# Optimization experiments

Hardware: AMD Instinct MI355X
Metric: run time of the kernel (lower is better)

## Reference

```python
import jax, jax.numpy as jnp
import numpy as np
from jax import lax

WIN_SIZE = 11
WIN_SIGMA = 1.5
DATA_RANGE = 1.0
K1, K2 = 0.01, 0.03


def _gauss_1d(win_size, sigma):
    coords = jnp.arange(win_size, dtype=jnp.float32) - win_size // 2
    g = jnp.exp(-(coords ** 2) / (2.0 * sigma ** 2))
    return g / jnp.sum(g)


def _gauss_filter(x, win):
    # Separable depthwise gaussian blur, VALID padding (matches pytorch_msssim).
    C = x.shape[1]
    kh = jnp.tile(win.reshape(1, 1, -1, 1), (C, 1, 1, 1))  # (C,1,k,1)
    kw = jnp.tile(win.reshape(1, 1, 1, -1), (C, 1, 1, 1))  # (C,1,1,k)
    dn = ('NCHW', 'OIHW', 'NCHW')
    x = lax.conv_general_dilated(x, kh, (1, 1), 'VALID',
                                 dimension_numbers=dn, feature_group_count=C)
    x = lax.conv_general_dilated(x, kw, (1, 1), 'VALID',
                                 dimension_numbers=dn, feature_group_count=C)
    return x


def _ssim(X, Y, win, data_range):
    C1 = (K1 * data_range) ** 2
    C2 = (K2 * data_range) ** 2
    mu1 = _gauss_filter(X, win)
    mu2 = _gauss_filter(Y, win)
    mu1_sq = mu1 * mu1
    mu2_sq = mu2 * mu2
    mu1_mu2 = mu1 * mu2
    sigma1_sq = _gauss_filter(X * X, win) - mu1_sq
    sigma2_sq = _gauss_filter(Y * Y, win) - mu2_sq
    sigma12 = _gauss_filter(X * Y, win) - mu1_mu2
    cs_map = (2.0 * sigma12 + C2) / (sigma1_sq + sigma2_sq + C2)
    ssim_map = ((2.0 * mu1_mu2 + C1) / (mu1_sq + mu2_sq + C1)) * cs_map
    return jnp.mean(ssim_map)


def setup_inputs() -> dict:
    key = jax.random.key(0)
    k1, k2 = jax.random.split(key)
    shape = (16, 3, 384, 512)
    pred = jax.random.uniform(k1, shape, dtype=jnp.float32)
    target = jax.random.uniform(k2, shape, dtype=jnp.float32)
    return {"pred": pred, "target": target}


def reference(pred, target):
    win = _gauss_1d(WIN_SIZE, WIN_SIGMA)
    ssim_val = _ssim(pred, target, win, DATA_RANGE)
    return 1.0 - ssim_val
```

## Files before the change

### kernel.cpp

```cpp
#include <hip/hip_runtime.h>
#include <math.h>

#define WIN 11
#define IMG_H 384
#define IMG_W 512
#define OUT_H (IMG_H - WIN + 1)
#define OUT_W (IMG_W - WIN + 1)
#define RPW 2
#define NPAIRS 187
#define NIMG 48
#define TOTAL_PAIRS (NPAIRS * NIMG)
#define WPB 4
#define NBLOCKS 2248
#define BPX 281
#define NBUCKETS 256

typedef float v2 __attribute__((ext_vector_type(2)));

struct GaussW { float g[WIN]; };
struct Row { float4 xa, xb, ya, yb; };

__device__ __forceinline__ v2 shfl_v2(v2 v, int src) {
    v2 r; r.x = __shfl(v.x, src, 64); r.y = __shfl(v.y, src, 64); return r;
}

__device__ __forceinline__ void horiz11_v2(const v2 (&A)[8], v2 (&out)[8],
                                           int lane, const GaussW& gw)
{
    v2 V[18];
    #pragma unroll
    for (int j = 0; j < 8; ++j) V[j] = A[j];
    #pragma unroll
    for (int j = 0; j < 8; ++j) V[8 + j] = shfl_v2(A[j], lane + 1);
    V[16] = shfl_v2(A[0], lane + 2);
    V[17] = shfl_v2(A[1], lane + 2);
    #pragma unroll
    for (int j = 0; j < 8; ++j) {
        v2 o = 0.f;
        #pragma unroll
        for (int k = 0; k < WIN; ++k) {
            v2 g = gw.g[k];
            o = __builtin_elementwise_fma(g, V[j + k], o);
        }
        out[j] = o;
    }
}

__device__ __forceinline__ void horiz11_f(const float (&A)[8], float (&out)[8],
                                          int lane, const GaussW& gw)
{
    float V[18];
    #pragma unroll
    for (int j = 0; j < 8; ++j) V[j] = A[j];
    #pragma unroll
    for (int j = 0; j < 8; ++j) V[8 + j] = __shfl(A[j], lane + 1, 64);
    V[16] = __shfl(A[0], lane + 2, 64);
    V[17] = __shfl(A[1], lane + 2, 64);
    #pragma unroll
    for (int j = 0; j < 8; ++j) {
        float o = 0.f;
        #pragma unroll
        for (int k = 0; k < WIN; ++k) o = fmaf(gw.g[k], V[j + k], o);
        out[j] = o;
    }
}

__global__ __launch_bounds__(256) void ssim_fused_kernel(
    const float* __restrict__ X, const float* __restrict__ Y,
    double* __restrict__ accum, GaussW gw)
{
    const int wave = threadIdx.x >> 6;
    const int lane = threadIdx.x & 63;

    const int id = blockIdx.x;
    const int wb = (id & 7) * BPX + (id >> 3);
    const int P  = wb * WPB + wave;
    if (P >= TOTAL_PAIRS) return;

    const int img  = P / NPAIRS;
    const int pair = P % NPAIRS;
    const int r0   = pair * RPW;
    const int c0   = lane << 3;
    const float* __restrict__ Xb = X + ((size_t)img * IMG_H + r0) * IMG_W + c0;
    const float* __restrict__ Yb = Y + ((size_t)img * IMG_H + r0) * IMG_W + c0;

    v2 a01[RPW][8], a23[RPW][8];
    float a4[RPW][8];
    #pragma unroll
    for (int r = 0; r < RPW; ++r)
        #pragma unroll
        for (int j = 0; j < 8; ++j) { a01[r][j] = 0.f; a23[r][j] = 0.f; a4[r][j] = 0.f; }

    #define LOADROW(B, K) {                                                  \
        const float* _rx = Xb + (size_t)(K) * IMG_W;                         \
        const float* _ry = Yb + (size_t)(K) * IMG_W;                         \
        (B).xa = *(const float4*)(_rx);                                      \
        (B).xb = *(const float4*)(_rx + 4);                                  \
        (B).ya = *(const float4*)(_ry);                                      \
        (B).yb = *(const float4*)(_ry + 4);                                  \
    }

    Row buf[3];
    LOADROW(buf[0], 0); LOADROW(buf[1], 1); LOADROW(buf[2], 2);
    __builtin_amdgcn_sched_barrier(0);

    #pragma unroll
    for (int k = 0; k < RPW + WIN - 1; ++k) {
        Row cur = buf[k % 3];
        if (k + 3 < RPW + WIN - 1) LOADROW(buf[k % 3], k + 3);

        v2 p[8] = {{cur.xa.x, cur.ya.x}, {cur.xa.y, cur.ya.y},
                   {cur.xa.z, cur.ya.z}, {cur.xa.w, cur.ya.w},
                   {cur.xb.x, cur.yb.x}, {cur.xb.y, cur.yb.y},
                   {cur.xb.z, cur.yb.z}, {cur.xb.w, cur.yb.w}};
        #pragma unroll
        for (int r = 0; r < RPW; ++r) {
            if (k - r >= 0 && k - r < WIN) {
                v2 g = gw.g[k - r];
                #pragma unroll
                for (int j = 0; j < 8; ++j) {
                    v2 q = p[j];
                    a01[r][j] = __builtin_elementwise_fma(g, q, a01[r][j]);
                    v2 t = g * q;
                    a23[r][j] = __builtin_elementwise_fma(t, q, a23[r][j]);
                    a4[r][j]  = fmaf(t.x, q.y, a4[r][j]);
                }
            }
        }
        __builtin_amdgcn_sched_barrier(0);
    }
    #undef LOADROW

    const float C1 = 1e-4f, C2 = 9e-4f;
    float sum = 0.f;
    #pragma unroll
    for (int r = 0; r < RPW; ++r) {
        v2 h01[8], h23[8];
        float h4[8];
        horiz11_v2(a01[r], h01, lane, gw);
        horiz11_v2(a23[r], h23, lane, gw);
        horiz11_f (a4[r],  h4,  lane, gw);
        #pragma unroll
        for (int j = 0; j < 8; ++j) {
            v2 mu = h01[j];
            v2 sq = mu * mu;
            float m12 = mu.x * mu.y;
            v2 sig = h23[j] - sq;
            float s12 = h4[j] - m12;
            float num = fmaf(2.f, m12, C1) * fmaf(2.f, s12, C2);
            float den = (sq.x + sq.y + C1) * (sig.x + sig.y + C2);
            float ssim = num * __builtin_amdgcn_rcpf(den);
            sum += (c0 + j < OUT_W) ? ssim : 0.f;
        }
    }

    #pragma unroll
    for (int off = 32; off; off >>= 1)
        sum += __shfl_down(sum, off, 64);
    if (lane == 0)
        atomicAdd(&accum[P & (NBUCKETS - 1)], (double)sum);
}

__global__ void ssim_finalize_kernel(const double* __restrict__ accum,
                                     float* __restrict__ out, double inv_count)
{
    const int lane = threadIdx.x;
    double s = 0.0;
    for (int i = lane; i < NBUCKETS; i += 64) s += accum[i];
    #pragma unroll
    for (int off = 32; off; off >>= 1)
        s += __shfl_down(s, off, 64);
    if (lane == 0) out[0] = (float)(1.0 - s * inv_count);
}

extern "C" void kernel_launch(void* const* d_in, const int* in_sizes, int n_in,
                              void* d_out, int out_size, void* d_ws, size_t ws_size,
                              hipStream_t stream) {
    const float* X = (const float*)d_in[0];
    const float* Y = (const float*)d_in[1];
    float* out = (float*)d_out;
    double* accum = (double*)d_ws;

    GaussW gw;
    {
        double g[WIN], ssum = 0.0;
        for (int i = 0; i < WIN; ++i) {
            double d = (double)i - WIN / 2;
            g[i] = exp(-(d * d) / (2.0 * 1.5 * 1.5));
            ssum += g[i];
        }
        for (int i = 0; i < WIN; ++i) gw.g[i] = (float)(g[i] / ssum);
    }

    hipMemsetAsync(accum, 0, NBUCKETS * sizeof(double), stream);

    ssim_fused_kernel<<<NBLOCKS, 64 * WPB, 0, stream>>>(X, Y, accum, gw);

    const double inv_count = 1.0 / ((double)NIMG * OUT_H * OUT_W);
    ssim_finalize_kernel<<<1, 64, 0, stream>>>(accum, out, inv_count);
}
```

Before: 123.6 us.

## Process three row-pairs per wave and prefetch next pair during horizontal pass

Each wave now loops over three consecutive row-pairs instead of one, with the grid shrunk to match. The first three rows of the next pair are loaded before the horizontal blur and SSIM math of the current pair, so load latency is hidden behind compute. Accumulators are initialised with a multiply on the first tap instead of zero-fill plus FMA. The cost is fewer waves in flight, a non-unrolled outer loop, and more live registers.

```diff
diff --git a/kernel.cpp b/kernel.cpp
--- a/kernel.cpp
+++ b/kernel.cpp
@@ -10,9 +10,10 @@
 #define NPAIRS 187
 #define NIMG 48
 #define TOTAL_PAIRS (NPAIRS * NIMG)
+#define PPW 3
 #define WPB 4
-#define NBLOCKS 2248
-#define BPX 281
+#define NBLOCKS 752
+#define BPX 94
 #define NBUCKETS 256
 
 typedef float v2 __attribute__((ext_vector_type(2)));
@@ -74,22 +75,8 @@
 
     const int id = blockIdx.x;
     const int wb = (id & 7) * BPX + (id >> 3);
-    const int P  = wb * WPB + wave;
-    if (P >= TOTAL_PAIRS) return;
-
-    const int img  = P / NPAIRS;
-    const int pair = P % NPAIRS;
-    const int r0   = pair * RPW;
-    const int c0   = lane << 3;
-    const float* __restrict__ Xb = X + ((size_t)img * IMG_H + r0) * IMG_W + c0;
-    const float* __restrict__ Yb = Y + ((size_t)img * IMG_H + r0) * IMG_W + c0;
-
-    v2 a01[RPW][8], a23[RPW][8];
-    float a4[RPW][8];
-    #pragma unroll
-    for (int r = 0; r < RPW; ++r)
-        #pragma unroll
-        for (int j = 0; j < 8; ++j) { a01[r][j] = 0.f; a23[r][j] = 0.f; a4[r][j] = 0.f; }
+    const int P0 = (wb * WPB + wave) * PPW;
+    const int c0 = lane << 3;
 
     #define LOADROW(B, K) {                                                  \
         const float* _rx = Xb + (size_t)(K) * IMG_W;                         \
@@ -99,66 +86,98 @@
         (B).ya = *(const float4*)(_ry);                                      \
         (B).yb = *(const float4*)(_ry + 4);                                  \
     }
-
+    #define PAIR_BASES(PC) {                                                 \
+        const int _img  = (PC) / NPAIRS;                                     \
+        const int _pair = (PC) - _img * NPAIRS;                              \
+        const int _r0   = _pair * RPW;                \
+        Xb = X + ((size_t)_img * IMG_H + _r0) * IMG_W + c0;                  \
+        Yb = Y + ((size_t)_img * IMG_H + _r0) * IMG_W + c0;                  \
+    }
+
+    const float* Xb; const float* Yb;
+    {
+        const int Pc = (P0 < TOTAL_PAIRS) ? P0 : (TOTAL_PAIRS - 1);
+        PAIR_BASES(Pc);
+    }
     Row buf[3];
     LOADROW(buf[0], 0); LOADROW(buf[1], 1); LOADROW(buf[2], 2);
     __builtin_amdgcn_sched_barrier(0);
 
-    #pragma unroll
-    for (int k = 0; k < RPW + WIN - 1; ++k) {
-        Row cur = buf[k % 3];
-        if (k + 3 < RPW + WIN - 1) LOADROW(buf[k % 3], k + 3);
-
-        v2 p[8] = {{cur.xa.x, cur.ya.x}, {cur.xa.y, cur.ya.y},
-                   {cur.xa.z, cur.ya.z}, {cur.xa.w, cur.ya.w},
-                   {cur.xb.x, cur.yb.x}, {cur.xb.y, cur.yb.y},
-                   {cur.xb.z, cur.yb.z}, {cur.xb.w, cur.yb.w}};
-        #pragma unroll
-        for (int r = 0; r < RPW; ++r) {
-            if (k - r >= 0 && k - r < WIN) {
-                v2 g = gw.g[k - r];
-                #pragma unroll
-                for (int j = 0; j < 8; ++j) {
-                    v2 q = p[j];
-                    a01[r][j] = __builtin_elementwise_fma(g, q, a01[r][j]);
-                    v2 t = g * q;
-                    a23[r][j] = __builtin_elementwise_fma(t, q, a23[r][j]);
-                    a4[r][j]  = fmaf(t.x, q.y, a4[r][j]);
+    for (int p = 0; p < PPW; ++p) {
+        v2 a01[RPW][8], a23[RPW][8];
+        float a4[RPW][8];
+
+        #pragma unroll
+        for (int k = 0; k < RPW + WIN - 1; ++k) {
+            Row cur = buf[k % 3];
+            if (k + 3 < RPW + WIN - 1) LOADROW(buf[k % 3], k + 3);
+
+            v2 pk[8] = {{cur.xa.x, cur.ya.x}, {cur.xa.y, cur.ya.y},
+                        {cur.xa.z, cur.ya.z}, {cur.xa.w, cur.ya.w},
+                        {cur.xb.x, cur.yb.x}, {cur.xb.y, cur.yb.y},
+                        {cur.xb.z, cur.yb.z}, {cur.xb.w, cur.yb.w}};
+            #pragma unroll
+            for (int r = 0; r < RPW; ++r) {
+                if (k - r >= 0 && k - r < WIN) {
+                    v2 g = gw.g[k - r];
+                    #pragma unroll
+                    for (int j = 0; j < 8; ++j) {
+                        v2 q = pk[j];
+                        v2 t = g * q;
+                        if (k == r) {
+                            a01[r][j] = t;
+                            a23[r][j] = t * q;
+                            a4[r][j]  = t.x * q.y;
+                        } else {
+                            a01[r][j] = __builtin_elementwise_fma(g, q, a01[r][j]);
+                            a23[r][j] = __builtin_elementwise_fma(t, q, a23[r][j]);
+                            a4[r][j]  = fmaf(t.x, q.y, a4[r][j]);
+                        }
+                    }
                 }
             }
+            __builtin_amdgcn_sched_barrier(0);
+        }
+
+        if (p + 1 < PPW) {
+            const int Pn = (P0 + p + 1 < TOTAL_PAIRS) ? (P0 + p + 1)
+                                                      : (TOTAL_PAIRS - 1);
+            PAIR_BASES(Pn);
+            LOADROW(buf[0], 0); LOADROW(buf[1], 1); LOADROW(buf[2], 2);
         }
         __builtin_amdgcn_sched_barrier(0);
+
+        const float C1 = 1e-4f, C2 = 9e-4f;
+        float sum = 0.f;
+        #pragma unroll
+        for (int r = 0; r < RPW; ++r) {
+            v2 h01[8], h23[8];
+            float h4[8];
+            horiz11_v2(a01[r], h01, lane, gw);
+            horiz11_v2(a23[r], h23, lane, gw);
+            horiz11_f (a4[r],  h4,  lane, gw);
+            #pragma unroll
+            for (int j = 0; j < 8; ++j) {
+                v2 mu = h01[j];
+                v2 sq = mu * mu;
+                float m12 = mu.x * mu.y;
+                v2 sig = h23[j] - sq;
+                float s12 = h4[j] - m12;
+                float num = fmaf(2.f, m12, C1) * fmaf(2.f, s12, C2);
+                float den = (sq.x + sq.y + C1) * (sig.x + sig.y + C2);
+                float ssim = num * __builtin_amdgcn_rcpf(den);
+                sum += (c0 + j < OUT_W) ? ssim : 0.f;
+            }
+        }
+
+        #pragma unroll
+        for (int off = 32; off; off >>= 1)
+            sum += __shfl_down(sum, off, 64);
+        if (lane == 0 && P0 + p < TOTAL_PAIRS)
+            atomicAdd(&accum[(P0 + p) & (NBUCKETS - 1)], (double)sum);
     }
     #undef LOADROW
-
-    const float C1 = 1e-4f, C2 = 9e-4f;
-    float sum = 0.f;
-    #pragma unroll
-    for (int r = 0; r < RPW; ++r) {
-        v2 h01[8], h23[8];
-        float h4[8];
-        horiz11_v2(a01[r], h01, lane, gw);
-        horiz11_v2(a23[r], h23, lane, gw);
-        horiz11_f (a4[r],  h4,  lane, gw);
-        #pragma unroll
-        for (int j = 0; j < 8; ++j) {
-            v2 mu = h01[j];
-            v2 sq = mu * mu;
-            float m12 = mu.x * mu.y;
-            v2 sig = h23[j] - sq;
-            float s12 = h4[j] - m12;
-            float num = fmaf(2.f, m12, C1) * fmaf(2.f, s12, C2);
-            float den = (sq.x + sq.y + C1) * (sig.x + sig.y + C2);
-            float ssim = num * __builtin_amdgcn_rcpf(den);
-            sum += (c0 + j < OUT_W) ? ssim : 0.f;
-        }
-    }
-
-    #pragma unroll
-    for (int off = 32; off; off >>= 1)
-        sum += __shfl_down(sum, off, 64);
-    if (lane == 0)
-        atomicAdd(&accum[P & (NBUCKETS - 1)], (double)sum);
+    #undef PAIR_BASES
 }
 
 __global__ void ssim_finalize_kernel(const double* __restrict__ accum,
```

Measured after the change: 146.9 us. +18.9%, slower.

## Deepen row prefetch, drop accumulator zeroing, write per-wave partials without memset

Applied to the files above, without the earlier changes.

The row prefetch ring buffer grows from 3 to 5 rows so more global loads are in flight. The first tap now initialises the accumulators directly instead of zeroing them and then adding. When the workspace is large enough, each wave writes its partial sum to its own slot instead of doing a double atomicAdd. That removes the memset launch, and a 256-thread finalize kernel reduces all the slots. The deeper buffer raises register pressure, and the finalize kernel must now read about 8.4K doubles instead of 256.

```diff
diff --git a/kernel.cpp b/kernel.cpp
--- a/kernel.cpp
+++ b/kernel.cpp
@@ -13,6 +13,7 @@
 #define WPB 4
 #define NBLOCKS 2248
 #define BPX 281
+#define NBUF 5
 #define NBUCKETS 256
 
 typedef float v2 __attribute__((ext_vector_type(2)));
@@ -67,7 +68,7 @@
 
 __global__ __launch_bounds__(256) void ssim_fused_kernel(
     const float* __restrict__ X, const float* __restrict__ Y,
-    double* __restrict__ accum, GaussW gw)
+    double* __restrict__ slots, GaussW gw, int flat)
 {
     const int wave = threadIdx.x >> 6;
     const int lane = threadIdx.x & 63;
@@ -86,10 +87,6 @@
 
     v2 a01[RPW][8], a23[RPW][8];
     float a4[RPW][8];
-    #pragma unroll
-    for (int r = 0; r < RPW; ++r)
-        #pragma unroll
-        for (int j = 0; j < 8; ++j) { a01[r][j] = 0.f; a23[r][j] = 0.f; a4[r][j] = 0.f; }
 
     #define LOADROW(B, K) {                                                  \
         const float* _rx = Xb + (size_t)(K) * IMG_W;                         \
@@ -100,30 +97,37 @@
         (B).yb = *(const float4*)(_ry + 4);                                  \
     }
 
-    Row buf[3];
-    LOADROW(buf[0], 0); LOADROW(buf[1], 1); LOADROW(buf[2], 2);
+    Row buf[NBUF];
+    #pragma unroll
+    for (int w = 0; w < NBUF; ++w) LOADROW(buf[w], w);
     __builtin_amdgcn_sched_barrier(0);
 
     #pragma unroll
     for (int k = 0; k < RPW + WIN - 1; ++k) {
-        Row cur = buf[k % 3];
-        if (k + 3 < RPW + WIN - 1) LOADROW(buf[k % 3], k + 3);
-
-        v2 p[8] = {{cur.xa.x, cur.ya.x}, {cur.xa.y, cur.ya.y},
-                   {cur.xa.z, cur.ya.z}, {cur.xa.w, cur.ya.w},
-                   {cur.xb.x, cur.yb.x}, {cur.xb.y, cur.yb.y},
-                   {cur.xb.z, cur.yb.z}, {cur.xb.w, cur.yb.w}};
+        Row cur = buf[k % NBUF];
+        if (k + NBUF < RPW + WIN - 1) LOADROW(buf[k % NBUF], k + NBUF);
+
+        v2 pk[8] = {{cur.xa.x, cur.ya.x}, {cur.xa.y, cur.ya.y},
+                    {cur.xa.z, cur.ya.z}, {cur.xa.w, cur.ya.w},
+                    {cur.xb.x, cur.yb.x}, {cur.xb.y, cur.yb.y},
+                    {cur.xb.z, cur.yb.z}, {cur.xb.w, cur.yb.w}};
         #pragma unroll
         for (int r = 0; r < RPW; ++r) {
             if (k - r >= 0 && k - r < WIN) {
                 v2 g = gw.g[k - r];
                 #pragma unroll
                 for (int j = 0; j < 8; ++j) {
-                    v2 q = p[j];
-                    a01[r][j] = __builtin_elementwise_fma(g, q, a01[r][j]);
+                    v2 q = pk[j];
                     v2 t = g * q;
-                    a23[r][j] = __builtin_elementwise_fma(t, q, a23[r][j]);
-                    a4[r][j]  = fmaf(t.x, q.y, a4[r][j]);
+                    if (k == r) {
+                        a01[r][j] = t;
+                        a23[r][j] = t * q;
+                        a4[r][j]  = t.x * q.y;
+                    } else {
+                        a01[r][j] = __builtin_elementwise_fma(g, q, a01[r][j]);
+                        a23[r][j] = __builtin_elementwise_fma(t, q, a23[r][j]);
+                        a4[r][j]  = fmaf(t.x, q.y, a4[r][j]);
+                    }
                 }
             }
         }
@@ -157,20 +161,28 @@
     #pragma unroll
     for (int off = 32; off; off >>= 1)
         sum += __shfl_down(sum, off, 64);
-    if (lane == 0)
-        atomicAdd(&accum[P & (NBUCKETS - 1)], (double)sum);
-}
-
-__global__ void ssim_finalize_kernel(const double* __restrict__ accum,
-                                     float* __restrict__ out, double inv_count)
-{
-    const int lane = threadIdx.x;
+    if (lane == 0) {
+        if (flat) slots[P] = (double)sum;
+        else atomicAdd(&slots[P & (NBUCKETS - 1)], (double)sum);
+    }
+}
+
+__global__ void ssim_finalize_kernel(const double* __restrict__ slots,
+                                     float* __restrict__ out,
+                                     double inv_count, int count)
+{
+    const int tid  = threadIdx.x;
+    const int wave = tid >> 6, lane = tid & 63;
+    __shared__ double ws[4];
     double s = 0.0;
-    for (int i = lane; i < NBUCKETS; i += 64) s += accum[i];
+    for (int i = tid; i < count; i += 256) s += slots[i];
     #pragma unroll
     for (int off = 32; off; off >>= 1)
         s += __shfl_down(s, off, 64);
-    if (lane == 0) out[0] = (float)(1.0 - s * inv_count);
+    if (lane == 0) ws[wave] = s;
+    __syncthreads();
+    if (tid == 0)
+        out[0] = (float)(1.0 - (ws[0] + ws[1] + ws[2] + ws[3]) * inv_count);
 }
 
 extern "C" void kernel_launch(void* const* d_in, const int* in_sizes, int n_in,
@@ -179,7 +191,7 @@
     const float* X = (const float*)d_in[0];
     const float* Y = (const float*)d_in[1];
     float* out = (float*)d_out;
-    double* accum = (double*)d_ws;
+    double* slots = (double*)d_ws;
 
     GaussW gw;
     {
@@ -192,10 +204,13 @@
         for (int i = 0; i < WIN; ++i) gw.g[i] = (float)(g[i] / ssum);
     }
 
-    hipMemsetAsync(accum, 0, NBUCKETS * sizeof(double), stream);
-
-    ssim_fused_kernel<<<NBLOCKS, 64 * WPB, 0, stream>>>(X, Y, accum, gw);
+    const int flat = (ws_size >= (size_t)TOTAL_PAIRS * sizeof(double)) ? 1 : 0;
+    if (!flat)
+        hipMemsetAsync(slots, 0, NBUCKETS * sizeof(double), stream);
+
+    ssim_fused_kernel<<<NBLOCKS, 64 * WPB, 0, stream>>>(X, Y, slots, gw, flat);
 
     const double inv_count = 1.0 / ((double)NIMG * OUT_H * OUT_W);
-    ssim_finalize_kernel<<<1, 64, 0, stream>>>(accum, out, inv_count);
-}
+    ssim_finalize_kernel<<<1, 256, 0, stream>>>(
+        slots, out, inv_count, flat ? TOTAL_PAIRS : NBUCKETS);
+}
```

Measured after the change: 130.3 us. 5.4% more time.
